# Kernel optimization log

Hardware: AMD Instinct MI355X
Metric: run time of the kernel (lower is better)

## Reference

```python
import jax, jax.numpy as jnp
import numpy as np

SPECIES = [1, 6, 7, 8]
N_SPECIES = len(SPECIES)
MAX_Z = max(SPECIES) + 1  # 9
N_IN = 256
N_HIDDEN = 512
N_OUT = 1
N_ATOMS = 65536


def setup_inputs() -> dict:
    key = jax.random.key(0)
    ks = jax.random.split(key, 9)
    x = jax.random.normal(ks[0], (N_ATOMS, N_IN), dtype=jnp.float32)
    z = jax.random.randint(ks[1], (N_ATOMS,), 0, MAX_Z)
    s = 0.05
    # Stacked per-species MLP parameters: [S, ...]
    W1 = jax.random.normal(ks[2], (N_SPECIES, N_HIDDEN, N_IN), dtype=jnp.float32) * s
    b1 = jax.random.normal(ks[3], (N_SPECIES, N_HIDDEN), dtype=jnp.float32) * s
    W2 = jax.random.normal(ks[4], (N_SPECIES, N_HIDDEN, N_HIDDEN), dtype=jnp.float32) * s
    b2 = jax.random.normal(ks[5], (N_SPECIES, N_HIDDEN), dtype=jnp.float32) * s
    W3 = jax.random.normal(ks[6], (N_SPECIES, N_OUT, N_HIDDEN), dtype=jnp.float32) * s
    b3 = jax.random.normal(ks[7], (N_SPECIES, N_OUT), dtype=jnp.float32) * s
    # One-hot embedding table [MAX_Z, N_SPECIES]: row Z has 1.0 at its species slot
    E = np.zeros((MAX_Z, N_SPECIES), dtype=np.float32)
    for idx, Z in enumerate(SPECIES):
        E[Z, idx] = 1.0
    E = jnp.asarray(E)
    return {"x": x, "z": z, "W1": W1, "b1": b1, "W2": W2, "b2": b2,
            "W3": W3, "b3": b3, "E": E}


def reference(x, z, W1, b1, W2, b2, W3, b3, E):
    # Every atom runs through all species MLPs (dense, O(N*S)), as in the original.
    # h1: [N, S, H]
    h1 = jnp.tanh(jnp.einsum('ni,shi->nsh', x, W1) + b1[None])
    h2 = jnp.tanh(jnp.einsum('nsh,sgh->nsg', h1, W2) + b2[None])
    # out_s: [N, S, n_out] -> [N, S*n_out] (n_out == 1 -> [N, S])
    out_s = (jnp.einsum('nsh,soh->nso', h2, W3) + b3[None]).reshape(x.shape[0], -1)
    gate = E[z]  # [N, S] embedding lookup (one-hot hard routing)
    return jnp.sum(out_s * gate, axis=1)  # [N]
```

## Files before the change

kernel.cpp:

```cpp
#include <hip/hip_runtime.h>

typedef __attribute__((ext_vector_type(8))) short bf16x8;
typedef __attribute__((ext_vector_type(4))) float f32x4;
typedef __attribute__((ext_vector_type(2))) unsigned int u32x2;
typedef unsigned short us;

#define NATOMS 65536
#define NIN 256
#define NHID 512
#define TM 64
#define LDBX 528
#define LDBH 1040

__device__ __forceinline__ us f2b(float f) {
    union { float f; unsigned int u; } a; a.f = f;
    unsigned int r = a.u + 0x7FFFu + ((a.u >> 16) & 1u);
    return (us)(r >> 16);
}
__device__ __forceinline__ float fast_tanh(float v) {
    float t = __builtin_amdgcn_exp2f(v * 2.88539008f);
    float r = __builtin_amdgcn_rcpf(t + 1.f);
    return __builtin_fmaf(-2.f, r, 1.f);
}
__device__ __forceinline__ unsigned cvt_pk(float lo, float hi) {
    unsigned p;
    asm("v_cvt_pk_bf16_f32 %0, %1, %2" : "=v"(p) : "v"(lo), "v"(hi));
    return p;
}

__global__ void cvt_kernel(const float* __restrict__ W1, const float* __restrict__ W2,
                           const float* __restrict__ W3,
                           us* __restrict__ W1p, us* __restrict__ W2p,
                           us* __restrict__ W3b) {
    int i = blockIdx.x * blockDim.x + threadIdx.x;
    if (i < 65536) {
        int s = i >> 14, rem = i & 16383;
        int ntile = rem >> 9, r2 = rem & 511;
        int kstep = r2 >> 6, lane = r2 & 63;
        int n = ntile * 16 + (lane & 15);
        int k = kstep * 32 + ((lane >> 4) << 3);
        const float* src = W1 + ((size_t)(s * NHID + n) * NIN + k);
        us p[8];
#pragma unroll
        for (int j = 0; j < 8; ++j) p[j] = f2b(src[j]);
        *(uint4*)(W1p + (size_t)i * 8) = *(uint4*)p;
    }
    if (i < 131072) {
        int s = i >> 15, rem = i & 32767;
        int ntile = rem >> 10, r2 = rem & 1023;
        int kstep = r2 >> 6, lane = r2 & 63;
        int n = ntile * 16 + (lane & 15);
        int k = kstep * 32 + ((lane >> 4) << 3);
        const float* src = W2 + ((size_t)(s * NHID + n) * NHID + k);
        us p[8];
#pragma unroll
        for (int j = 0; j < 8; ++j) p[j] = f2b(src[j]);
        *(uint4*)(W2p + (size_t)i * 8) = *(uint4*)p;
    }
    if (i < 2048) W3b[i] = f2b(W3[i]);
}

__global__ __launch_bounds__(1024) void compact_kernel(
    const int* __restrict__ z, int* __restrict__ cnt,
    int* __restrict__ lists, float* __restrict__ out) {
    __shared__ int lcnt[4];
    __shared__ int gbase[4];
    __shared__ int wbase[16][4];

    int tid = threadIdx.x;
    int wv = tid >> 6;
    int lane = tid & 63;
    if (tid < 4) lcnt[tid] = 0;
    __syncthreads();

    int i = blockIdx.x * 1024 + tid;
    int zz = z[i];
    int s = (zz == 1) ? 0 : (zz == 6) ? 1 : (zz == 7) ? 2 : (zz == 8) ? 3 : -1;
    if (s < 0) out[i] = 0.f;

    int prefix = 0;
#pragma unroll
    for (int sp = 0; sp < 4; ++sp) {
        unsigned long long m = __ballot(s == sp);
        if (m) {
            int c = __popcll(m);
            int leader = __ffsll((long long)m) - 1;
            if (lane == leader) wbase[wv][sp] = atomicAdd(&lcnt[sp], c);
            if (s == sp) prefix = __popcll(m & ((1ull << lane) - 1ull));
        }
    }
    __syncthreads();
    if (tid < 4) gbase[tid] = atomicAdd(&cnt[tid], lcnt[tid]);
    __syncthreads();

    if (s >= 0) lists[s * NATOMS + gbase[s] + wbase[wv][s] + prefix] = i;
}

template<int K, int LDB>
__device__ __forceinline__ void gemm_pass(const char* lds, const us* Wp,
                                          int lane, int wtile, f32x4 acc[4][2]) {
    constexpr int KS = K / 32;
    const us* wp0 = Wp + (((size_t)(wtile + 0) * KS) * 64 + lane) * 8;
    const us* wp1 = Wp + (((size_t)(wtile + 1) * KS) * 64 + lane) * 8;
    int aoff[4];
#pragma unroll
    for (int mt = 0; mt < 4; ++mt)
        aoff[mt] = (mt * 16 + (lane & 15)) * LDB + (((lane >> 4) << 3) << 1);

    bf16x8 a[2][4], b0[2], b1[2];
#pragma unroll
    for (int mt = 0; mt < 4; ++mt) a[0][mt] = *(const bf16x8*)(lds + aoff[mt]);
    b0[0] = *(const bf16x8*)wp0;
    b1[0] = *(const bf16x8*)wp1;

#pragma unroll
    for (int i = 0; i < KS; ++i) {
        const int cur = i & 1, nxt = cur ^ 1;
        if (i + 1 < KS) {
#pragma unroll
            for (int mt = 0; mt < 4; ++mt)
                a[nxt][mt] = *(const bf16x8*)(lds + aoff[mt] + (i + 1) * 64);
            b0[nxt] = *(const bf16x8*)(wp0 + (i + 1) * 512);
            b1[nxt] = *(const bf16x8*)(wp1 + (i + 1) * 512);
        }
#pragma unroll
        for (int mt = 0; mt < 4; ++mt)
            acc[mt][0] = __builtin_amdgcn_mfma_f32_16x16x32_bf16(a[cur][mt], b0[cur], acc[mt][0], 0, 0, 0);
#pragma unroll
        for (int mt = 0; mt < 4; ++mt)
            acc[mt][1] = __builtin_amdgcn_mfma_f32_16x16x32_bf16(a[cur][mt], b1[cur], acc[mt][1], 0, 0, 0);
    }
}

template<int LDB>
__device__ __forceinline__ void act_store(char* ldsOut, const float* __restrict__ bias,
                                          int lane, int ncb, f32x4 acc[4][2]) {
#pragma unroll
    for (int nt = 0; nt < 2; ++nt) {
        int n = ncb + nt * 16 + (lane & 15);
        float bv = bias[n];
#pragma unroll
        for (int mt = 0; mt < 4; ++mt) {
            float t0 = fast_tanh(acc[mt][nt][0] + bv);
            float t1 = fast_tanh(acc[mt][nt][1] + bv);
            float t2 = fast_tanh(acc[mt][nt][2] + bv);
            float t3 = fast_tanh(acc[mt][nt][3] + bv);
            unsigned p01 = cvt_pk(t0, t1);
            unsigned p23 = cvt_pk(t2, t3);
            int row0 = mt * 16 + ((lane >> 4) << 2);
            char* base = ldsOut + row0 * LDB + n * 2;
            *(us*)(base)           = (us)p01;
            *(us*)(base + LDB)     = (us)(p01 >> 16);
            *(us*)(base + 2 * LDB) = (us)p23;
            *(us*)(base + 3 * LDB) = (us)(p23 >> 16);
        }
    }
}

__global__ __launch_bounds__(512, 2) void mlp_kernel(
    const float* __restrict__ x, const int* __restrict__ cnt, const int* __restrict__ lists,
    const us* __restrict__ W1p, const us* __restrict__ W2p, const us* __restrict__ W3b,
    const float* __restrict__ b1, const float* __restrict__ b2, const float* __restrict__ b3,
    float* __restrict__ out) {
    int bx = blockIdx.x;
    int s = bx & 3;
    int t = bx >> 2;
    int base = t * TM;
    int n_s = cnt[s];
    if (base >= n_s) return;
    const int* list = lists + s * NATOMS;
    int cnt_t = n_s - base; if (cnt_t > TM) cnt_t = TM;

    __shared__ __align__(16) char ldsX[TM * LDBX];
    __shared__ __align__(16) char ldsH[TM * LDBH];

    int tid = threadIdx.x;
    int lane = tid & 63;
    int w = tid >> 6;

    {
        int r = tid >> 3;
        int cb = (tid & 7) * 32;
        int atom = (r < cnt_t) ? list[base + r] : -1;
        const float* xr = x + (size_t)(atom < 0 ? 0 : atom) * NIN;
#pragma unroll
        for (int j = 0; j < 8; ++j) {
            int c = cb + j * 4;
            float4 v;
            if (atom >= 0) v = *(const float4*)(xr + c);
            else v = make_float4(0.f, 0.f, 0.f, 0.f);
            u32x2 p;
            p.x = cvt_pk(v.x, v.y);
            p.y = cvt_pk(v.z, v.w);
            *(u32x2*)(ldsX + r * LDBX + c * 2) = p;
        }
    }
    __syncthreads();

#pragma unroll
    for (int h = 0; h < 2; ++h) {
        f32x4 acc[4][2];
#pragma unroll
        for (int i = 0; i < 4; ++i)
#pragma unroll
            for (int j = 0; j < 2; ++j) acc[i][j] = (f32x4){0.f, 0.f, 0.f, 0.f};
        gemm_pass<NIN, LDBX>(ldsX, W1p + (size_t)s * NHID * NIN, lane, w * 4 + h * 2, acc);
        act_store<LDBH>(ldsH, b1 + s * NHID, lane, w * 64 + h * 32, acc);
    }
    __syncthreads();

#pragma unroll
    for (int h = 0; h < 2; ++h) {
        f32x4 acc[4][2];
#pragma unroll
        for (int i = 0; i < 4; ++i)
#pragma unroll
            for (int j = 0; j < 2; ++j) acc[i][j] = (f32x4){0.f, 0.f, 0.f, 0.f};
        gemm_pass<NHID, LDBH>(ldsH, W2p + (size_t)s * NHID * NHID, lane, h * 16 + w * 2, acc);
        if (h == 0) {
            act_store<LDBX>(ldsX, b2 + s * NHID, lane, w * 32, acc);
        } else {
            __syncthreads();
            act_store<LDBH>(ldsH, b2 + s * NHID, lane, 256 + w * 32, acc);
        }
    }
    __syncthreads();

    {
        int m = tid >> 3;
        int q = tid & 7;
        const us* W3s = W3b + (size_t)s * NHID;
        float sum = 0.f;
#pragma unroll
        for (int j = 0; j < 8; ++j) {
            int hh = q * 64 + j * 8;
            bf16x8 hv;
            if (hh < 256) hv = *(const bf16x8*)(ldsX + m * LDBX + hh * 2);
            else          hv = *(const bf16x8*)(ldsH + m * LDBH + hh * 2);
            bf16x8 wv = *(const bf16x8*)(W3s + hh);
#pragma unroll
            for (int e = 0; e < 8; ++e) {
                union { unsigned u; float f; } ha, wa;
                ha.u = ((unsigned)(us)hv[e]) << 16;
                wa.u = ((unsigned)(us)wv[e]) << 16;
                sum += ha.f * wa.f;
            }
        }
        sum += __shfl_xor(sum, 1);
        sum += __shfl_xor(sum, 2);
        sum += __shfl_xor(sum, 4);
        if (q == 0 && m < cnt_t) out[list[base + m]] = sum + b3[s];
    }
}

extern "C" void kernel_launch(void* const* d_in, const int* in_sizes, int n_in,
                              void* d_out, int out_size, void* d_ws, size_t ws_size,
                              hipStream_t stream) {
    const float* x  = (const float*)d_in[0];
    const int*   z  = (const int*)d_in[1];
    const float* W1 = (const float*)d_in[2];
    const float* b1 = (const float*)d_in[3];
    const float* W2 = (const float*)d_in[4];
    const float* b2 = (const float*)d_in[5];
    const float* W3 = (const float*)d_in[6];
    const float* b3 = (const float*)d_in[7];
    float* out = (float*)d_out;

    char* ws = (char*)d_ws;
    int* cnt = (int*)ws;
    int* lists = (int*)(ws + 256);
    us* W1p = (us*)(ws + 256 + (size_t)4 * NATOMS * 4);
    us* W2p = W1p + 4 * NHID * NIN;
    us* W3b = W2p + 4 * NHID * NHID;

    (void)hipMemsetAsync(cnt, 0, 16, stream);
    cvt_kernel<<<512, 256, 0, stream>>>(W1, W2, W3, W1p, W2p, W3b);
    compact_kernel<<<NATOMS / 1024, 1024, 0, stream>>>(z, cnt, lists, out);
    mlp_kernel<<<4096, 512, 0, stream>>>(x, cnt, lists, W1p, W2p, W3b, b1, b2, b3, out);
}
```

Baseline: 63.88 us.

## Widen per-wave MFMA tile to 64 columns in a single GEMM pass

Each wave now computes a 64x64 output tile (four N-subtiles) in one pass instead of two passes of 32 columns. A-fragments from LDS are reused across four B tiles, halving LDS reads per MFMA. Layer-2 output goes back into the hidden buffer after a barrier rather than being split across two buffers. Launch bounds drop to one block per CU to allow the larger accumulator register footprint, which cuts occupancy and latency hiding.

New measurement: 61.99 us. 3.0% less time.

```diff
diff --git a/kernel.cpp b/kernel.cpp
--- a/kernel.cpp
+++ b/kernel.cpp
@@ -97,21 +97,23 @@
 }
 
 template<int K, int LDB>
-__device__ __forceinline__ void gemm_pass(const char* lds, const us* Wp,
-                                          int lane, int wtile, f32x4 acc[4][2]) {
+__device__ __forceinline__ void gemm4(const char* lds, const us* Wp,
+                                      int lane, int wtile, f32x4 acc[4][4]) {
     constexpr int KS = K / 32;
-    const us* wp0 = Wp + (((size_t)(wtile + 0) * KS) * 64 + lane) * 8;
-    const us* wp1 = Wp + (((size_t)(wtile + 1) * KS) * 64 + lane) * 8;
+    const us* wp[4];
+#pragma unroll
+    for (int nt = 0; nt < 4; ++nt)
+        wp[nt] = Wp + (((size_t)(wtile + nt) * KS) * 64 + lane) * 8;
     int aoff[4];
 #pragma unroll
     for (int mt = 0; mt < 4; ++mt)
         aoff[mt] = (mt * 16 + (lane & 15)) * LDB + (((lane >> 4) << 3) << 1);
 
-    bf16x8 a[2][4], b0[2], b1[2];
+    bf16x8 a[2][4], b[2][4];
 #pragma unroll
     for (int mt = 0; mt < 4; ++mt) a[0][mt] = *(const bf16x8*)(lds + aoff[mt]);
-    b0[0] = *(const bf16x8*)wp0;
-    b1[0] = *(const bf16x8*)wp1;
+#pragma unroll
+    for (int nt = 0; nt < 4; ++nt) b[0][nt] = *(const bf16x8*)wp[nt];
 
 #pragma unroll
     for (int i = 0; i < KS; ++i) {
@@ -120,23 +122,23 @@
 #pragma unroll
             for (int mt = 0; mt < 4; ++mt)
                 a[nxt][mt] = *(const bf16x8*)(lds + aoff[mt] + (i + 1) * 64);
-            b0[nxt] = *(const bf16x8*)(wp0 + (i + 1) * 512);
-            b1[nxt] = *(const bf16x8*)(wp1 + (i + 1) * 512);
-        }
-#pragma unroll
-        for (int mt = 0; mt < 4; ++mt)
-            acc[mt][0] = __builtin_amdgcn_mfma_f32_16x16x32_bf16(a[cur][mt], b0[cur], acc[mt][0], 0, 0, 0);
-#pragma unroll
-        for (int mt = 0; mt < 4; ++mt)
-            acc[mt][1] = __builtin_amdgcn_mfma_f32_16x16x32_bf16(a[cur][mt], b1[cur], acc[mt][1], 0, 0, 0);
+#pragma unroll
+            for (int nt = 0; nt < 4; ++nt)
+                b[nxt][nt] = *(const bf16x8*)(wp[nt] + (i + 1) * 512);
+        }
+#pragma unroll
+        for (int nt = 0; nt < 4; ++nt)
+#pragma unroll
+            for (int mt = 0; mt < 4; ++mt)
+                acc[mt][nt] = __builtin_amdgcn_mfma_f32_16x16x32_bf16(a[cur][mt], b[cur][nt], acc[mt][nt], 0, 0, 0);
     }
 }
 
 template<int LDB>
 __device__ __forceinline__ void act_store(char* ldsOut, const float* __restrict__ bias,
-                                          int lane, int ncb, f32x4 acc[4][2]) {
-#pragma unroll
-    for (int nt = 0; nt < 2; ++nt) {
+                                          int lane, int ncb, f32x4 acc[4][4]) {
+#pragma unroll
+    for (int nt = 0; nt < 4; ++nt) {
         int n = ncb + nt * 16 + (lane & 15);
         float bv = bias[n];
 #pragma unroll
@@ -157,7 +159,7 @@
     }
 }
 
-__global__ __launch_bounds__(512, 2) void mlp_kernel(
+__global__ __launch_bounds__(512, 1) void mlp_kernel(
     const float* __restrict__ x, const int* __restrict__ cnt, const int* __restrict__ lists,
     const us* __restrict__ W1p, const us* __restrict__ W2p, const us* __restrict__ W3b,
     const float* __restrict__ b1, const float* __restrict__ b2, const float* __restrict__ b3,
@@ -177,6 +179,8 @@
     int tid = threadIdx.x;
     int lane = tid & 63;
     int w = tid >> 6;
+    int wtile = w * 4;
+    int ncb = w * 64;
 
     {
         int r = tid >> 3;
@@ -197,32 +201,26 @@
     }
     __syncthreads();
 
-#pragma unroll
-    for (int h = 0; h < 2; ++h) {
-        f32x4 acc[4][2];
+    {
+        f32x4 acc[4][4];
 #pragma unroll
         for (int i = 0; i < 4; ++i)
 #pragma unroll
-            for (int j = 0; j < 2; ++j) acc[i][j] = (f32x4){0.f, 0.f, 0.f, 0.f};
-        gemm_pass<NIN, LDBX>(ldsX, W1p + (size_t)s * NHID * NIN, lane, w * 4 + h * 2, acc);
-        act_store<LDBH>(ldsH, b1 + s * NHID, lane, w * 64 + h * 32, acc);
-    }
-    __syncthreads();
-
-#pragma unroll
-    for (int h = 0; h < 2; ++h) {
-        f32x4 acc[4][2];
+            for (int j = 0; j < 4; ++j) acc[i][j] = (f32x4){0.f, 0.f, 0.f, 0.f};
+        gemm4<NIN, LDBX>(ldsX, W1p + (size_t)s * NHID * NIN, lane, wtile, acc);
+        act_store<LDBH>(ldsH, b1 + s * NHID, lane, ncb, acc);
+    }
+    __syncthreads();
+
+    {
+        f32x4 acc[4][4];
 #pragma unroll
         for (int i = 0; i < 4; ++i)
 #pragma unroll
-            for (int j = 0; j < 2; ++j) acc[i][j] = (f32x4){0.f, 0.f, 0.f, 0.f};
-        gemm_pass<NHID, LDBH>(ldsH, W2p + (size_t)s * NHID * NHID, lane, h * 16 + w * 2, acc);
-        if (h == 0) {
-            act_store<LDBX>(ldsX, b2 + s * NHID, lane, w * 32, acc);
-        } else {
-            __syncthreads();
-            act_store<LDBH>(ldsH, b2 + s * NHID, lane, 256 + w * 32, acc);
-        }
+            for (int j = 0; j < 4; ++j) acc[i][j] = (f32x4){0.f, 0.f, 0.f, 0.f};
+        gemm4<NHID, LDBH>(ldsH, W2p + (size_t)s * NHID * NHID, lane, wtile, acc);
+        __syncthreads();
+        act_store<LDBH>(ldsH, b2 + s * NHID, lane, ncb, acc);
     }
     __syncthreads();
 
@@ -234,9 +232,7 @@
 #pragma unroll
         for (int j = 0; j < 8; ++j) {
             int hh = q * 64 + j * 8;
-            bf16x8 hv;
-            if (hh < 256) hv = *(const bf16x8*)(ldsX + m * LDBX + hh * 2);
-            else          hv = *(const bf16x8*)(ldsH + m * LDBH + hh * 2);
+            bf16x8 hv = *(const bf16x8*)(ldsH + m * LDBH + hh * 2);
             bf16x8 wv = *(const bf16x8*)(W3s + hh);
 #pragma unroll
             for (int e = 0; e < 8; ++e) {
```
